# Kernel tuning notes

Hardware: AMD Instinct MI355X
Metric: run time of the kernel (lower is better)

Reference implementation:

```python
import jax, jax.numpy as jnp
import numpy as np

B, IN, OUT, P, NS = 256, 1024, 512, 1000, 128

def setup_inputs() -> dict:
    key = jax.random.key(0)
    ks = jax.random.split(key, 6)
    return {
        "x": jax.random.normal(ks[0], (B, IN), jnp.float32),
        "noise": jax.random.normal(ks[1], (B, NS, P), jnp.float32),
        "fb_w": jax.random.normal(ks[2], (1, IN), jnp.float32) * (1.0 / np.sqrt(IN)),
        "fb_b": jnp.zeros((1,), jnp.float32),
        "decay_param": jnp.full((1,), 0.1, jnp.float32),
        "conv_w": jax.random.normal(ks[3], (P, P, 3), jnp.float32) * (1.0 / np.sqrt(3 * P)),
        "conv_b": jnp.zeros((P,), jnp.float32),
        "out_w": jax.random.normal(ks[4], (OUT, P), jnp.float32) * (1.0 / np.sqrt(P)),
        "out_b": jnp.zeros((OUT,), jnp.float32),
    }


def reference(x, noise, fb_w, fb_b, decay_param, conv_w, conv_b, out_w, out_b):
    # x: [B, IN]; noise: [B, NS, P] (Brownian increments for the SDE kernel)
    n_steps = noise.shape[1]
    dt = 1.0 / n_steps                       # T = 1.0
    sd = jnp.sqrt(jnp.asarray(dt, x.dtype))
    # per-sample feedback value: sigmoid(feedback_controller(x))
    feedback = jax.nn.sigmoid(x @ fb_w.T + fb_b)            # [B, 1]
    # decay value: sigmoid(decay_controller) * 0.5 (scalar)
    decay = jax.nn.sigmoid(decay_param[0]) * 0.5
    retain = 1.0 - decay * dt
    # Batched Euler-Maruyama Brownian SDE: X_{t+1} = (1 - decay*dt) X_t + feedback*sqrt(dt)*eps_t
    eps = jnp.transpose(noise, (1, 0, 2))                    # [NS, B, P]
    x0 = jnp.zeros((x.shape[0], noise.shape[2]), x.dtype)

    def step(X, e):
        Xn = X * retain + feedback * sd * e
        return Xn, Xn

    _, paths = jax.lax.scan(step, x0, eps)                   # [NS, B, P]
    paths_bct = jnp.transpose(paths, (1, 2, 0))              # [B, P, NS]
    # temporal_aggregator: Conv1d(P, P, kernel=3, padding=1) over time, then mean over time
    agg = jax.lax.conv_general_dilated(
        paths_bct, conv_w, window_strides=(1,), padding=[(1, 1)],
        dimension_numbers=("NCH", "OIH", "NCH"))
    agg = (agg + conv_b[None, :, None]).mean(axis=2)         # [B, P]
    # output_projection: P -> OUT
    return agg @ out_w.T + out_b
```

## Files before the change

### kernel.cpp

```cpp
#include <hip/hip_runtime.h>
#include <hip/hip_bf16.h>

#define B_N   256
#define IN_N  1024
#define OUT_N 512
#define P_N   1000
#define NS_N  128

#define K1P   3072
#define N1P   1024
#define K2P   1024
#define SK    16

typedef __attribute__((ext_vector_type(8))) short short8v;
typedef __attribute__((ext_vector_type(4))) float f32x4;
typedef unsigned short ushort_t;

__device__ __forceinline__ float sigmoid_f(float z) { return 1.0f / (1.0f + __expf(-z)); }

__device__ __forceinline__ void split1(float x, ushort_t& h, ushort_t& l) {
    __hip_bfloat16 hb = __float2bfloat16(x);
    float r = x - __bfloat162float(hb);
    __hip_bfloat16 lb = __float2bfloat16(r);
    h = __bfloat16_as_ushort(hb);
    l = __bfloat16_as_ushort(lb);
}

__device__ __forceinline__ void split8(float4 v0, float4 v1, short8v& h, short8v& l) {
    float vv[8] = {v0.x, v0.y, v0.z, v0.w, v1.x, v1.y, v1.z, v1.w};
    #pragma unroll
    for (int j = 0; j < 8; ++j) {
        ushort_t hh, ll;
        split1(vv[j], hh, ll);
        h[j] = (short)hh;
        l[j] = (short)ll;
    }
}

__global__ __launch_bounds__(256) void sde_fused_kernel(const float* __restrict__ x,
                                                        const float* __restrict__ fb_w,
                                                        const float* __restrict__ fb_b,
                                                        const float* __restrict__ noise,
                                                        const float* __restrict__ decay_param,
                                                        ushort_t* __restrict__ Thi,
                                                        ushort_t* __restrict__ Tlo) {
    int b = blockIdx.x;
    int chunk = blockIdx.y;
    int t = threadIdx.x;

    float4 xv = ((const float4*)(x + (size_t)b * IN_N))[t];
    float4 wv = ((const float4*)fb_w)[t];
    float s = xv.x * wv.x + xv.y * wv.y + xv.z * wv.z + xv.w * wv.w;
    __shared__ float red[256];
    red[t] = s;
    __syncthreads();
    for (int off = 128; off >= 1; off >>= 1) {
        if (t < off) red[t] += red[t + off];
        __syncthreads();
    }
    float fbv = sigmoid_f(red[0] + fb_b[0]);

    float decay = sigmoid_f(decay_param[0]) * 0.5f;
    const float dt = 1.0f / NS_N;
    float retain = 1.0f - decay * dt;
    float inv_omr = 1.0f / (decay * dt);

    int c0 = chunk * 512 + t * 2;
    bool act = (c0 < P_N);
    const float* base = noise + (size_t)b * NS_N * P_N + (act ? c0 : 0);

    float sE0 = 0.f, sE1 = 0.f, L0 = 0.f, L1 = 0.f, F0 = 0.f, F1 = 0.f;
    float rp = 1.0f;
    #pragma unroll 8
    for (int s_ = NS_N - 1; s_ >= 0; --s_) {
        float2 e = *(const float2*)(base + (size_t)s_ * P_N);
        sE0 += e.x; sE1 += e.y;
        L0 += rp * e.x; L1 += rp * e.y;
        if (s_ == 0) { F0 = e.x; F1 = e.y; }
        rp *= retain;
    }

    float sd = sqrtf(dt);
    float scale = act ? (fbv * sd * (1.0f / NS_N)) : 0.0f;
    size_t tb = (size_t)b * K1P + 3 * (size_t)c0;
    float Ls[2] = {L0, L1}, Ss[2] = {sE0, sE1}, Fs[2] = {F0, F1};
    #pragma unroll
    for (int j = 0; j < 2; ++j) {
        float Aj = (Ss[j] - retain * Ls[j]) * inv_omr;
        float t0 = scale * (Aj - Ls[j]);
        float t1 = scale * Aj;
        float t2 = scale * (Aj - Fs[j]);
        ushort_t h, l;
        split1(t0, h, l); Thi[tb + 3 * j + 0] = h; Tlo[tb + 3 * j + 0] = l;
        split1(t1, h, l); Thi[tb + 3 * j + 1] = h; Tlo[tb + 3 * j + 1] = l;
        split1(t2, h, l); Thi[tb + 3 * j + 2] = h; Tlo[tb + 3 * j + 2] = l;
    }
}

__global__ __launch_bounds__(512) void gemm_hilo_mfma(const ushort_t* __restrict__ Ahi,
                                                      const ushort_t* __restrict__ Alo,
                                                      const float* __restrict__ B,
                                                      float* __restrict__ Cpart,
                                                      int lda, int ldb,
                                                      int Nvalid, int Kvalid,
                                                      int Kper, int ldc) {
    __shared__ __align__(16) ushort_t As_hi[128 * 64];
    __shared__ __align__(16) ushort_t As_lo[128 * 64];
    __shared__ __align__(16) ushort_t Bs_hi[128 * 64];
    __shared__ __align__(16) ushort_t Bs_lo[128 * 64];

    const int tid  = threadIdx.x;
    const int lane = tid & 63;
    const int wave = tid >> 6;
    const int r15  = lane & 15;
    const int g4   = lane >> 4;
    const int wrow = wave >> 2;
    const int wcol = wave & 3;
    const int n0 = blockIdx.x * 128;
    const int m0 = blockIdx.y * 128;
    const size_t kbeg = (size_t)blockIdx.z * Kper;

    f32x4 acc[4][2] = {};

    for (int kt = 0; kt < Kper; kt += 64) {
        const size_t kk0 = kbeg + kt;
        #pragma unroll
        for (int c = 0; c < 2; ++c) {
            int chunk = tid + c * 512;
            int row = chunk >> 3;
            int g   = chunk & 7;
            int ldsoff = row * 64 + ((g ^ (row & 7)) << 3);

            const size_t ka = (size_t)(m0 + row) * lda + kk0 + g * 8;
            *(short8v*)&As_hi[ldsoff] = *(const short8v*)(Ahi + ka);
            *(short8v*)&As_lo[ldsoff] = *(const short8v*)(Alo + ka);

            float4 b0 = {0, 0, 0, 0}, b1 = {0, 0, 0, 0};
            if ((n0 + row) < Nvalid && (int)(kk0 + g * 8) < Kvalid) {
                const float* bp = B + (size_t)(n0 + row) * ldb + kk0 + g * 8;
                b0 = *(const float4*)bp;
                b1 = *(const float4*)(bp + 4);
            }
            short8v bh, bl;
            split8(b0, b1, bh, bl);
            *(short8v*)&Bs_hi[ldsoff] = bh;
            *(short8v*)&Bs_lo[ldsoff] = bl;
        }
        __syncthreads();

        #pragma unroll
        for (int ks = 0; ks < 2; ++ks) {
            const int g = ks * 4 + g4;
            short8v ah[4], al[4], bh[2], bl[2];
            #pragma unroll
            for (int f = 0; f < 4; ++f) {
                int arow = wrow * 64 + f * 16 + r15;
                int aoff = arow * 64 + ((g ^ (arow & 7)) << 3);
                ah[f] = *(const short8v*)&As_hi[aoff];
                al[f] = *(const short8v*)&As_lo[aoff];
            }
            #pragma unroll
            for (int f = 0; f < 2; ++f) {
                int brow = wcol * 32 + f * 16 + r15;
                int boff = brow * 64 + ((g ^ (brow & 7)) << 3);
                bh[f] = *(const short8v*)&Bs_hi[boff];
                bl[f] = *(const short8v*)&Bs_lo[boff];
            }
            #pragma unroll
            for (int mf = 0; mf < 4; ++mf) {
                #pragma unroll
                for (int nf = 0; nf < 2; ++nf) {
                    acc[mf][nf] = __builtin_amdgcn_mfma_f32_16x16x32_bf16(ah[mf], bh[nf], acc[mf][nf], 0, 0, 0);
                    acc[mf][nf] = __builtin_amdgcn_mfma_f32_16x16x32_bf16(ah[mf], bl[nf], acc[mf][nf], 0, 0, 0);
                    acc[mf][nf] = __builtin_amdgcn_mfma_f32_16x16x32_bf16(al[mf], bh[nf], acc[mf][nf], 0, 0, 0);
                }
            }
        }
        __syncthreads();
    }

    float* cp = Cpart + (size_t)blockIdx.z * 256 * ldc;
    #pragma unroll
    for (int mf = 0; mf < 4; ++mf) {
        #pragma unroll
        for (int nf = 0; nf < 2; ++nf) {
            #pragma unroll
            for (int r = 0; r < 4; ++r) {
                int m = m0 + wrow * 64 + mf * 16 + g4 * 4 + r;
                int n = n0 + wcol * 32 + nf * 16 + r15;
                cp[(size_t)m * ldc + n] = acc[mf][nf][r];
            }
        }
    }
}

__global__ __launch_bounds__(256) void reduce_agg_kernel(const float* __restrict__ Cpart,
                                                         const float* __restrict__ conv_b,
                                                         ushort_t* __restrict__ agg_hi,
                                                         ushort_t* __restrict__ agg_lo) {
    int idx = blockIdx.x * 256 + threadIdx.x;
    int n = idx & (N1P - 1);
    float s = 0.f;
    if (n < P_N) {
        s = conv_b[n];
        #pragma unroll
        for (int z = 0; z < SK; ++z) s += Cpart[(size_t)z * (B_N * N1P) + idx];
    }
    ushort_t h, l;
    split1(s, h, l);
    agg_hi[idx] = h;
    agg_lo[idx] = l;
}

__global__ __launch_bounds__(256) void reduce_out_kernel(const float* __restrict__ Cpart,
                                                         const float* __restrict__ out_b,
                                                         float* __restrict__ out) {
    int idx = blockIdx.x * 256 + threadIdx.x;
    int n = idx & (OUT_N - 1);
    float s = out_b[n];
    #pragma unroll
    for (int z = 0; z < SK; ++z) s += Cpart[(size_t)z * (B_N * OUT_N) + idx];
    out[idx] = s;
}

extern "C" void kernel_launch(void* const* d_in, const int* in_sizes, int n_in,
                              void* d_out, int out_size, void* d_ws, size_t ws_size,
                              hipStream_t stream) {
    const float* x           = (const float*)d_in[0];
    const float* noise       = (const float*)d_in[1];
    const float* fb_w        = (const float*)d_in[2];
    const float* fb_b        = (const float*)d_in[3];
    const float* decay_param = (const float*)d_in[4];
    const float* conv_w      = (const float*)d_in[5];
    const float* conv_b      = (const float*)d_in[6];
    const float* out_w       = (const float*)d_in[7];
    const float* out_b       = (const float*)d_in[8];
    float* out = (float*)d_out;

    char* ws = (char*)d_ws;
    size_t off = 0;
    ushort_t* Thi   = (ushort_t*)(ws + off); off += (size_t)B_N * K1P * 2;
    ushort_t* Tlo   = (ushort_t*)(ws + off); off += (size_t)B_N * K1P * 2;
    ushort_t* AgHi  = (ushort_t*)(ws + off); off += (size_t)B_N * K2P * 2;
    ushort_t* AgLo  = (ushort_t*)(ws + off); off += (size_t)B_N * K2P * 2;
    float*    Cpart = (float*)(ws + off);    off += (size_t)SK * B_N * N1P * 4;

    {
        dim3 grid(B_N, 2);
        sde_fused_kernel<<<grid, 256, 0, stream>>>(x, fb_w, fb_b, noise, decay_param, Thi, Tlo);
    }

    {
        dim3 grid(N1P / 128, B_N / 128, SK);
        gemm_hilo_mfma<<<grid, 512, 0, stream>>>(Thi, Tlo, conv_w, Cpart,
                                                 K1P, 3 * P_N, P_N, 3 * P_N,
                                                 K1P / SK, N1P);
        reduce_agg_kernel<<<(B_N * N1P) / 256, 256, 0, stream>>>(Cpart, conv_b, AgHi, AgLo);
    }

    {
        dim3 grid(OUT_N / 128, B_N / 128, SK);
        gemm_hilo_mfma<<<grid, 512, 0, stream>>>(AgHi, AgLo, out_w, Cpart,
                                                 K2P, P_N, OUT_N, P_N,
                                                 K2P / SK, OUT_N);
        reduce_out_kernel<<<(B_N * OUT_N) / 256, 256, 0, stream>>>(Cpart, out_b, out);
    }
}
```

Measured before the change: 53.40 us.

## Drop hi/lo bf16 split to single bf16 GEMMs and rework SDE reduction

Replaces the three-MFMA hi/lo split-bf16 emulation of fp32 GEMM with plain single bf16 operands, which cuts MFMA work and shared-memory/global traffic by roughly a third or more. The SDE kernel now processes four columns per thread with float4 loads and splits the time dimension across two thread halves, combined through shared memory. The second GEMM uses a smaller split-K factor. Dropping the low-order correction lowers accuracy and may exceed tolerance.

```diff
diff --git a/kernel.cpp b/kernel.cpp
--- a/kernel.cpp
+++ b/kernel.cpp
@@ -10,7 +10,8 @@
 #define K1P   3072
 #define N1P   1024
 #define K2P   1024
-#define SK    16
+#define SK1   16
+#define SK2   8
 
 typedef __attribute__((ext_vector_type(8))) short short8v;
 typedef __attribute__((ext_vector_type(4))) float f32x4;
@@ -18,23 +19,8 @@
 
 __device__ __forceinline__ float sigmoid_f(float z) { return 1.0f / (1.0f + __expf(-z)); }
 
-__device__ __forceinline__ void split1(float x, ushort_t& h, ushort_t& l) {
-    __hip_bfloat16 hb = __float2bfloat16(x);
-    float r = x - __bfloat162float(hb);
-    __hip_bfloat16 lb = __float2bfloat16(r);
-    h = __bfloat16_as_ushort(hb);
-    l = __bfloat16_as_ushort(lb);
-}
-
-__device__ __forceinline__ void split8(float4 v0, float4 v1, short8v& h, short8v& l) {
-    float vv[8] = {v0.x, v0.y, v0.z, v0.w, v1.x, v1.y, v1.z, v1.w};
-    #pragma unroll
-    for (int j = 0; j < 8; ++j) {
-        ushort_t hh, ll;
-        split1(vv[j], hh, ll);
-        h[j] = (short)hh;
-        l[j] = (short)ll;
-    }
+__device__ __forceinline__ ushort_t f2bf(float x) {
+    return __bfloat16_as_ushort(__float2bfloat16(x));
 }
 
 __global__ __launch_bounds__(256) void sde_fused_kernel(const float* __restrict__ x,
@@ -42,11 +28,12 @@
                                                         const float* __restrict__ fb_b,
                                                         const float* __restrict__ noise,
                                                         const float* __restrict__ decay_param,
-                                                        ushort_t* __restrict__ Thi,
-                                                        ushort_t* __restrict__ Tlo) {
-    int b = blockIdx.x;
-    int chunk = blockIdx.y;
-    int t = threadIdx.x;
+                                                        ushort_t* __restrict__ Thi) {
+    const int b  = blockIdx.x;
+    const int ch = blockIdx.y;
+    const int t  = threadIdx.x;
+    const int cg = t & 127;
+    const int th = t >> 7;
 
     float4 xv = ((const float4*)(x + (size_t)b * IN_N))[t];
     float4 wv = ((const float4*)fb_w)[t];
@@ -64,50 +51,62 @@
     const float dt = 1.0f / NS_N;
     float retain = 1.0f - decay * dt;
     float inv_omr = 1.0f / (decay * dt);
-
-    int c0 = chunk * 512 + t * 2;
-    bool act = (c0 < P_N);
-    const float* base = noise + (size_t)b * NS_N * P_N + (act ? c0 : 0);
-
-    float sE0 = 0.f, sE1 = 0.f, L0 = 0.f, L1 = 0.f, F0 = 0.f, F1 = 0.f;
-    float rp = 1.0f;
-    #pragma unroll 8
-    for (int s_ = NS_N - 1; s_ >= 0; --s_) {
-        float2 e = *(const float2*)(base + (size_t)s_ * P_N);
-        sE0 += e.x; sE1 += e.y;
-        L0 += rp * e.x; L1 += rp * e.y;
-        if (s_ == 0) { F0 = e.x; F1 = e.y; }
-        rp *= retain;
-    }
-
-    float sd = sqrtf(dt);
-    float scale = act ? (fbv * sd * (1.0f / NS_N)) : 0.0f;
-    size_t tb = (size_t)b * K1P + 3 * (size_t)c0;
-    float Ls[2] = {L0, L1}, Ss[2] = {sE0, sE1}, Fs[2] = {F0, F1};
-    #pragma unroll
-    for (int j = 0; j < 2; ++j) {
-        float Aj = (Ss[j] - retain * Ls[j]) * inv_omr;
-        float t0 = scale * (Aj - Ls[j]);
-        float t1 = scale * Aj;
-        float t2 = scale * (Aj - Fs[j]);
-        ushort_t h, l;
-        split1(t0, h, l); Thi[tb + 3 * j + 0] = h; Tlo[tb + 3 * j + 0] = l;
-        split1(t1, h, l); Thi[tb + 3 * j + 1] = h; Tlo[tb + 3 * j + 1] = l;
-        split1(t2, h, l); Thi[tb + 3 * j + 2] = h; Tlo[tb + 3 * j + 2] = l;
-    }
-}
-
-__global__ __launch_bounds__(512) void gemm_hilo_mfma(const ushort_t* __restrict__ Ahi,
-                                                      const ushort_t* __restrict__ Alo,
+    float r2 = retain * retain, r4 = r2 * r2, r8 = r4 * r4;
+    float r16 = r8 * r8, r32 = r16 * r16, r64 = r32 * r32;
+
+    const int c0 = ch * 512 + cg * 4;
+    const bool act = (c0 < P_N);
+
+    float4 sE = {0, 0, 0, 0}, L = {0, 0, 0, 0}, F = {0, 0, 0, 0};
+    if (act) {
+        const float* base = noise + (size_t)b * NS_N * P_N + c0;
+        const int s0 = th * 64;
+        float rp = 1.0f;
+        #pragma unroll 16
+        for (int ss = s0 + 63; ss >= s0; --ss) {
+            float4 e = *(const float4*)(base + (size_t)ss * P_N);
+            sE.x += e.x; sE.y += e.y; sE.z += e.z; sE.w += e.w;
+            L.x += rp * e.x; L.y += rp * e.y; L.z += rp * e.z; L.w += rp * e.w;
+            if (ss == 0) F = e;
+            rp *= retain;
+        }
+    }
+
+    __shared__ float4 xSE[128], xL[128], xF[128];
+    if (th == 0) { xSE[cg] = sE; xL[cg] = L; xF[cg] = F; }
+    __syncthreads();
+
+    if (th == 1) {
+        size_t tb = (size_t)b * K1P + 3 * (size_t)c0;
+        if (!act) {
+            #pragma unroll
+            for (int j = 0; j < 12; ++j) Thi[tb + j] = 0;
+            return;
+        }
+        float4 se0 = xSE[cg], ll0 = xL[cg], ff = xF[cg];
+        float Se[4] = {se0.x + sE.x, se0.y + sE.y, se0.z + sE.z, se0.w + sE.w};
+        float Lv[4] = {L.x + r64 * ll0.x, L.y + r64 * ll0.y, L.z + r64 * ll0.z, L.w + r64 * ll0.w};
+        float Fv[4] = {ff.x, ff.y, ff.z, ff.w};
+        float sd = sqrtf(dt);
+        float scale = fbv * sd * (1.0f / NS_N);
+        #pragma unroll
+        for (int j = 0; j < 4; ++j) {
+            float Aj = (Se[j] - retain * Lv[j]) * inv_omr;
+            Thi[tb + 3 * j + 0] = f2bf(scale * (Aj - Lv[j]));
+            Thi[tb + 3 * j + 1] = f2bf(scale * Aj);
+            Thi[tb + 3 * j + 2] = f2bf(scale * (Aj - Fv[j]));
+        }
+    }
+}
+
+__global__ __launch_bounds__(512) void gemm_bf16_mfma(const ushort_t* __restrict__ A,
                                                       const float* __restrict__ B,
                                                       float* __restrict__ Cpart,
                                                       int lda, int ldb,
                                                       int Nvalid, int Kvalid,
                                                       int Kper, int ldc) {
-    __shared__ __align__(16) ushort_t As_hi[128 * 64];
-    __shared__ __align__(16) ushort_t As_lo[128 * 64];
-    __shared__ __align__(16) ushort_t Bs_hi[128 * 64];
-    __shared__ __align__(16) ushort_t Bs_lo[128 * 64];
+    __shared__ __align__(16) ushort_t As[128 * 64];
+    __shared__ __align__(16) ushort_t Bs[128 * 64];
 
     const int tid  = threadIdx.x;
     const int lane = tid & 63;
@@ -132,54 +131,48 @@
             int ldsoff = row * 64 + ((g ^ (row & 7)) << 3);
 
             const size_t ka = (size_t)(m0 + row) * lda + kk0 + g * 8;
-            *(short8v*)&As_hi[ldsoff] = *(const short8v*)(Ahi + ka);
-            *(short8v*)&As_lo[ldsoff] = *(const short8v*)(Alo + ka);
-
-            float4 b0 = {0, 0, 0, 0}, b1 = {0, 0, 0, 0};
+            *(short8v*)&As[ldsoff] = *(const short8v*)(A + ka);
+
+            short8v bh = {0, 0, 0, 0, 0, 0, 0, 0};
             if ((n0 + row) < Nvalid && (int)(kk0 + g * 8) < Kvalid) {
                 const float* bp = B + (size_t)(n0 + row) * ldb + kk0 + g * 8;
-                b0 = *(const float4*)bp;
-                b1 = *(const float4*)(bp + 4);
-            }
-            short8v bh, bl;
-            split8(b0, b1, bh, bl);
-            *(short8v*)&Bs_hi[ldsoff] = bh;
-            *(short8v*)&Bs_lo[ldsoff] = bl;
+                float4 b0 = *(const float4*)bp;
+                float4 b1 = *(const float4*)(bp + 4);
+                bh[0] = (short)f2bf(b0.x); bh[1] = (short)f2bf(b0.y);
+                bh[2] = (short)f2bf(b0.z); bh[3] = (short)f2bf(b0.w);
+                bh[4] = (short)f2bf(b1.x); bh[5] = (short)f2bf(b1.y);
+                bh[6] = (short)f2bf(b1.z); bh[7] = (short)f2bf(b1.w);
+            }
+            *(short8v*)&Bs[ldsoff] = bh;
         }
         __syncthreads();
 
         #pragma unroll
         for (int ks = 0; ks < 2; ++ks) {
             const int g = ks * 4 + g4;
-            short8v ah[4], al[4], bh[2], bl[2];
+            short8v af[4], bf_[2];
             #pragma unroll
             for (int f = 0; f < 4; ++f) {
                 int arow = wrow * 64 + f * 16 + r15;
-                int aoff = arow * 64 + ((g ^ (arow & 7)) << 3);
-                ah[f] = *(const short8v*)&As_hi[aoff];
-                al[f] = *(const short8v*)&As_lo[aoff];
+                af[f] = *(const short8v*)&As[arow * 64 + ((g ^ (arow & 7)) << 3)];
             }
             #pragma unroll
             for (int f = 0; f < 2; ++f) {
                 int brow = wcol * 32 + f * 16 + r15;
-                int boff = brow * 64 + ((g ^ (brow & 7)) << 3);
-                bh[f] = *(const short8v*)&Bs_hi[boff];
-                bl[f] = *(const short8v*)&Bs_lo[boff];
+                bf_[f] = *(const short8v*)&Bs[brow * 64 + ((g ^ (brow & 7)) << 3)];
             }
             #pragma unroll
             for (int mf = 0; mf < 4; ++mf) {
                 #pragma unroll
                 for (int nf = 0; nf < 2; ++nf) {
-                    acc[mf][nf] = __builtin_amdgcn_mfma_f32_16x16x32_bf16(ah[mf], bh[nf], acc[mf][nf], 0, 0, 0);
-                    acc[mf][nf] = __builtin_amdgcn_mfma_f32_16x16x32_bf16(ah[mf], bl[nf], acc[mf][nf], 0, 0, 0);
-                    acc[mf][nf] = __builtin_amdgcn_mfma_f32_16x16x32_bf16(al[mf], bh[nf], acc[mf][nf], 0, 0, 0);
+                    acc[mf][nf] = __builtin_amdgcn_mfma_f32_16x16x32_bf16(af[mf], bf_[nf], acc[mf][nf], 0, 0, 0);
                 }
             }
         }
         __syncthreads();
     }
 
-    float* cp = Cpart + (size_t)blockIdx.z * 256 * ldc;
+    float* cp = Cpart + (size_t)blockIdx.z * B_N * ldc;
     #pragma unroll
     for (int mf = 0; mf < 4; ++mf) {
         #pragma unroll
@@ -194,32 +187,28 @@
     }
 }
 
-__global__ __launch_bounds__(256) void reduce_agg_kernel(const float* __restrict__ Cpart,
+__global__ __launch_bounds__(256) void reduce_agg_kernel(const float* __restrict__ Cpart1,
                                                          const float* __restrict__ conv_b,
-                                                         ushort_t* __restrict__ agg_hi,
-                                                         ushort_t* __restrict__ agg_lo) {
+                                                         ushort_t* __restrict__ agg) {
     int idx = blockIdx.x * 256 + threadIdx.x;
     int n = idx & (N1P - 1);
     float s = 0.f;
     if (n < P_N) {
         s = conv_b[n];
         #pragma unroll
-        for (int z = 0; z < SK; ++z) s += Cpart[(size_t)z * (B_N * N1P) + idx];
-    }
-    ushort_t h, l;
-    split1(s, h, l);
-    agg_hi[idx] = h;
-    agg_lo[idx] = l;
-}
-
-__global__ __launch_bounds__(256) void reduce_out_kernel(const float* __restrict__ Cpart,
+        for (int z = 0; z < SK1; ++z) s += Cpart1[(size_t)z * (B_N * N1P) + idx];
+    }
+    agg[idx] = f2bf(s);
+}
+
+__global__ __launch_bounds__(256) void reduce_out_kernel(const float* __restrict__ Cpart2,
                                                          const float* __restrict__ out_b,
                                                          float* __restrict__ out) {
     int idx = blockIdx.x * 256 + threadIdx.x;
     int n = idx & (OUT_N - 1);
     float s = out_b[n];
     #pragma unroll
-    for (int z = 0; z < SK; ++z) s += Cpart[(size_t)z * (B_N * OUT_N) + idx];
+    for (int z = 0; z < SK2; ++z) s += Cpart2[(size_t)z * (B_N * OUT_N) + idx];
     out[idx] = s;
 }
 
@@ -239,30 +228,31 @@
 
     char* ws = (char*)d_ws;
     size_t off = 0;
-    ushort_t* Thi   = (ushort_t*)(ws + off); off += (size_t)B_N * K1P * 2;
-    ushort_t* Tlo   = (ushort_t*)(ws + off); off += (size_t)B_N * K1P * 2;
-    ushort_t* AgHi  = (ushort_t*)(ws + off); off += (size_t)B_N * K2P * 2;
-    ushort_t* AgLo  = (ushort_t*)(ws + off); off += (size_t)B_N * K2P * 2;
-    float*    Cpart = (float*)(ws + off);    off += (size_t)SK * B_N * N1P * 4;
+    ushort_t* Thi    = (ushort_t*)(ws + off); off += (size_t)B_N * K1P * 2;
+    ushort_t* agg    = (ushort_t*)(ws + off); off += (size_t)B_N * K2P * 2;
+    float*    Cpart1 = (float*)(ws + off);    off += (size_t)SK1 * B_N * N1P * 4;
+    float*    Cpart2 = (float*)(ws + off);    off += (size_t)SK2 * B_N * OUT_N * 4;
 
     {
         dim3 grid(B_N, 2);
-        sde_fused_kernel<<<grid, 256, 0, stream>>>(x, fb_w, fb_b, noise, decay_param, Thi, Tlo);
+        sde_fused_kernel<<<grid, 256, 0, stream>>>(x, fb_w, fb_b, noise, decay_param, Thi);
     }
 
     {
-        dim3 grid(N1P / 128, B_N / 128, SK);
-        gemm_hilo_mfma<<<grid, 512, 0, stream>>>(Thi, Tlo, conv_w, Cpart,
+        dim3 grid(N1P / 128, B_N / 128, SK1);
+        gemm_bf16_mfma<<<grid, 512, 0, stream>>>(Thi, conv_w, Cpart1,
                                                  K1P, 3 * P_N, P_N, 3 * P_N,
-                                                 K1P / SK, N1P);
-        reduce_agg_kernel<<<(B_N * N1P) / 256, 256, 0, stream>>>(Cpart, conv_b, AgHi, AgLo);
-    }
+                                                 K1P / SK1, N1P);
+    }
+
+    reduce_agg_kernel<<<(B_N * N1P) / 256, 256, 0, stream>>>(Cpart1, conv_b, agg);
 
     {
-        dim3 grid(OUT_N / 128, B_N / 128, SK);
-        gemm_hilo_mfma<<<grid, 512, 0, stream>>>(AgHi, AgLo, out_w, Cpart,
+        dim3 grid(OUT_N / 128, B_N / 128, SK2);
+        gemm_bf16_mfma<<<grid, 512, 0, stream>>>(agg, out_w, Cpart2,
                                                  K2P, P_N, OUT_N, P_N,
-                                                 K2P / SK, OUT_N);
-        reduce_out_kernel<<<(B_N * OUT_N) / 256, 256, 0, stream>>>(Cpart, out_b, out);
-    }
-}
+                                                 K2P / SK2, OUT_N);
+    }
+
+    reduce_out_kernel<<<(B_N * OUT_N) / 256, 256, 0, stream>>>(Cpart2, out_b, out);
+}
```

Result: no change. 52.60 us (-1.5%).
